# Performance work log

Measured on AMD Instinct MI355X. Metric: run time of the kernel, lower is better.

The kernel has to match this reference:

```python
import jax, jax.numpy as jnp
import numpy as np

TOPK = 5
LAMBDA_ALIGN_K = 16.0
MOM = 0.9          # EMA momentum
DEFAULT_SCORE = 0.5  # EMA bank default (bank starts empty)
EPS = 1e-8
NEG = 1.0e9


def pairwise_cosine(X):
    # torch F.normalize: X / max(||X||, eps)
    n = jnp.linalg.norm(X, axis=-1, keepdims=True)
    Xn = X / jnp.maximum(n, EPS)
    sim = Xn @ Xn.T
    return jnp.clip(sim, -1.0 + EPS, 1.0 - EPS)


def knn_mask(sim, allowed_base, topk=TOPK):
    B = sim.shape[0]
    eye = jnp.eye(B, dtype=sim.dtype)
    allowed = allowed_base * (1.0 - eye)
    masked = sim - NEG * eye
    masked = jnp.where(allowed < 0.5, -NEG, masked)
    masked = jnp.where(masked < 0.0, -NEG, masked)
    cand = (masked > 0).sum(axis=1)
    k = min(topk, max(B - 1, 1))
    keep_row = (cand >= topk).astype(sim.dtype)
    keep = keep_row[:, None] * keep_row[None, :]
    idx = jax.lax.top_k(masked, k)[1]                       # [B, k]
    M = jnp.zeros_like(sim).at[jnp.arange(B)[:, None], idx].set(1.0)
    M = jnp.maximum(M, M.T)
    return M * allowed * keep


def build_intra(sim, same, topk=TOPK):
    M = knn_mask(sim, same, topk)
    A = jnp.maximum(sim * M, 0.0) * same
    return A, M


def pga_loss(feats_sub, labels_sub):
    # feats_sub: [L, b, d]
    L = feats_sub.shape[0]
    same = (labels_sub[:, None] == labels_sub[None, :]).astype(jnp.float32)
    sims = jax.vmap(pairwise_cosine)(feats_sub)             # [L, b, b]
    A, M = jax.vmap(lambda s: build_intra(s, same))(sims)   # [L, b, b] each

    # EMA degree-based scores (no-grad in original; bank starts empty so
    # fetch-after-update == mom*default + (1-mom)*score_cur)
    S_intra = jnp.maximum(sims * same, 0.0)
    deg = jnp.maximum((S_intra > 0).sum(axis=2).astype(jnp.float32), 1.0)
    score_cur = jax.nn.sigmoid(S_intra.sum(axis=2) / deg)   # [L, b]
    ema = jax.lax.stop_gradient(MOM * DEFAULT_SCORE + (1.0 - MOM) * score_cur)

    # layer-pair masked MSE alignment, target detached
    A_deep = A[1:]
    A_tgt = jax.lax.stop_gradient(A[:-1])
    M_eff = jnp.maximum(M[:-1], M[1:])                      # [L-1, b, b]
    W = ema[:-1, :, None] * ema[:-1, None, :]               # [L-1, b, b]
    diff2 = (A_deep - A_tgt) ** 2 * W
    num = (diff2 * M_eff).sum(axis=(1, 2))
    den = jnp.maximum((M_eff * W).sum(axis=(1, 2)), EPS)
    terms = jnp.where(M_eff.sum(axis=(1, 2)) > 0, num / den, 0.0)
    raw = terms.sum() / max(L - 1, 1)
    return LAMBDA_ALIGN_K * raw


def setup_inputs() -> dict:
    key = jax.random.key(0)
    k1, k2 = jax.random.split(key)
    feats_final = jax.random.normal(k1, (8, 2048, 512), dtype=jnp.float32)
    labels = jax.random.randint(k2, (2048,), 0, 128).astype(jnp.int64)
    sample_ids = jnp.arange(2048, dtype=jnp.int64)
    return {"feats_final": feats_final, "labels": labels, "sample_ids": sample_ids}


def reference(feats_final, labels, sample_ids):
    # candidate subset from last layer (no-grad in original)
    X_last = feats_final[-1]
    S_last = pairwise_cosine(X_last)
    same_full = (labels[:, None] == labels[None, :]).astype(jnp.float32)
    _, M_last = build_intra(S_last, same_full)
    cand_mask = (M_last > 0).sum(axis=1) > 0
    idx_sub = jnp.nonzero(cand_mask)[0]  # eager (concrete) subselection
    feats_sub = feats_final[:, idx_sub]  # [L, b, d]
    labels_sub = labels[idx_sub]
    return pga_loss(feats_sub, labels_sub)
```

## Files before the change

kernel.cpp:

```cpp
#include <hip/hip_runtime.h>
#include <cmath>

#define NB   2048
#define ND   512
#define NL   8
#define NLAB 128
#define MAXM 64
#define TOPK_ 5
#define NTH  256
#define MAXSLOT 9
#define GSTRIDE (MAXM*MAXM)

#define SLOT_DECL(s) int off##s = -1; int lds##s = 0; float4 pre##s;
#define SLOT_INIT(s) { int idx = tid + (s)*NTH; if (idx < (m << 5)) { \
    int i = idx >> 5, k4 = idx & 31; \
    off##s = (g_s[i] << 9) + (k4 << 2); \
    lds##s = i * 132 + (k4 << 2); \
    pre##s = *(const float4*)(X + off##s); } }
#define SLOT_STORE(s) if (off##s >= 0) *(float4*)(XtF + lds##s) = pre##s;
#define SLOT_FETCH(s, kcn) if (off##s >= 0) pre##s = *(const float4*)(X + off##s + (kcn));

__global__ __launch_bounds__(NTH) void k_gram(
    const float* __restrict__ feats, const int* __restrict__ labels,
    float* __restrict__ G, int* __restrict__ cnt,
    unsigned long long* __restrict__ insub)
{
    __shared__ int wsum[4];
    __shared__ int g_s[MAXM];
    __shared__ float Xt[MAXM][132];
    __shared__ float rinvp[64];
    __shared__ unsigned long long tops_s[64];
    __shared__ unsigned char keep_s[64];
    float* XtF = &Xt[0][0];
    int c = blockIdx.x, l = blockIdx.y, tid = threadIdx.x;
    int lane = tid & 63, wv = tid >> 6;

    int my[8]; int n = 0; int base_i = tid * 8;
    for (int t = 0; t < 8; ++t) {
        int i = base_i + t;
        if (labels[i] == c) my[n++] = i;
    }
    int scan = n;
    #pragma unroll
    for (int off = 1; off < 64; off <<= 1) {
        int v = __shfl_up(scan, off);
        if (lane >= off) scan += v;
    }
    if (lane == 63) wsum[wv] = scan;
    __syncthreads();
    int w0 = wsum[0], w1 = wsum[1], w2 = wsum[2], w3 = wsum[3];
    int m = w0 + w1 + w2 + w3; if (m > MAXM) m = MAXM;
    int base = (wv > 0 ? w0 : 0) + (wv > 1 ? w1 : 0) + (wv > 2 ? w2 : 0);
    int excl = base + scan - n;
    for (int t = 0; t < n; ++t) {
        int slot = excl + t;
        if (slot < MAXM) g_s[slot] = my[t];
    }
    if (l == 0 && tid == 0) cnt[c] = m;
    __syncthreads();
    if (m == 0) {
        if (l == 7 && tid == 0) insub[c] = 0ull;
        return;
    }

    const float* X = feats + (size_t)l * NB * ND;

    SLOT_DECL(0) SLOT_DECL(1) SLOT_DECL(2) SLOT_DECL(3)
    SLOT_DECL(4) SLOT_DECL(5) SLOT_DECL(6) SLOT_DECL(7)
    SLOT_INIT(0) SLOT_INIT(1) SLOT_INIT(2) SLOT_INIT(3)
    SLOT_INIT(4) SLOT_INIT(5) SLOT_INIT(6) SLOT_INIT(7)

    const int P = m * (m + 1) / 2;
    float acc0[MAXSLOT], acc1[MAXSLOT];
    short is_[MAXSLOT], js_[MAXSLOT];
    int ns = 0;
    for (int p = tid; p < P; p += NTH) {
        int i = (int)((sqrtf(8.0f * (float)p + 1.0f) - 1.0f) * 0.5f);
        while (((i + 1) * (i + 2)) / 2 <= p) ++i;
        while ((i * (i + 1)) / 2 > p) --i;
        is_[ns] = (short)i;
        js_[ns] = (short)(p - (i * (i + 1)) / 2);
        acc0[ns] = 0.0f; acc1[ns] = 0.0f;
        ++ns;
    }

    for (int kc = 0; kc < ND; kc += 128) {
        if (kc) __syncthreads();
        SLOT_STORE(0) SLOT_STORE(1) SLOT_STORE(2) SLOT_STORE(3)
        SLOT_STORE(4) SLOT_STORE(5) SLOT_STORE(6) SLOT_STORE(7)
        __syncthreads();
        if (kc + 128 < ND) {
            int kcn = kc + 128;
            SLOT_FETCH(0, kcn) SLOT_FETCH(1, kcn) SLOT_FETCH(2, kcn) SLOT_FETCH(3, kcn)
            SLOT_FETCH(4, kcn) SLOT_FETCH(5, kcn) SLOT_FETCH(6, kcn) SLOT_FETCH(7, kcn)
        }
        for (int s = 0; s < ns; ++s) {
            int i = is_[s], j = js_[s];
            float a0 = acc0[s], a1 = acc1[s];
            #pragma unroll
            for (int k4 = 0; k4 < 32; ++k4) {
                float4 a = *(const float4*)&Xt[i][k4 << 2];
                float4 b = *(const float4*)&Xt[j][k4 << 2];
                a0 = fmaf(a.x, b.x, a0); a1 = fmaf(a.y, b.y, a1);
                a0 = fmaf(a.z, b.z, a0); a1 = fmaf(a.w, b.w, a1);
            }
            acc0[s] = a0; acc1[s] = a1;
        }
    }

    float (*Gs)[65] = (float(*)[65])(&Xt[0][0]);
    __syncthreads();
    for (int s = 0; s < ns; ++s) {
        int i = is_[s], j = js_[s];
        float v = acc0[s] + acc1[s];
        Gs[i][j] = v; Gs[j][i] = v;
    }
    if (tid < m) for (int j = m; j < 64; ++j) Gs[tid][j] = -2.0f;
    __syncthreads();
    if (tid < 64) rinvp[tid] = (tid < m) ? 1.0f / fmaxf(sqrtf(Gs[tid][tid]), 1e-8f) : 0.0f;
    __syncthreads();
    for (int idx = tid; idx < (m << 6); idx += NTH) {
        int i = idx >> 6, j = idx & 63;
        if (j < m) {
            float raw = Gs[i][j];
            Gs[i][j] = fminf(fmaxf(raw * rinvp[i] * rinvp[j], -1.0f), 1.0f);
        }
    }
    __syncthreads();
    float* Gc = G + ((size_t)l * NLAB + c) * GSTRIDE;
    for (int idx4 = tid; idx4 < (m << 4); idx4 += NTH) {
        int i = idx4 >> 4, j0 = (idx4 & 15) << 2;
        *(float4*)(Gc + i * MAXM + j0) = *(const float4*)&Gs[i][j0];
    }
    if (l != 7) return;

    if (tid < 64) { keep_s[tid] = 0; tops_s[tid] = 0ull; }
    __syncthreads();
    unsigned long long tops = 0ull; bool keep = false;
    if (tid < m) {
        float v0=-1.f,v1=-1.f,v2=-1.f,v3=-1.f,v4=-1.f;
        int i0=0,i1=0,i2=0,i3=0,i4=0, cand=0;
        #pragma unroll 8
        for (int j = 0; j < 64; ++j) {
            float v = Gs[tid][j];
            if (v > 0.0f && j != tid) {
                ++cand;
                if      (v > v0) { v4=v3;i4=i3; v3=v2;i3=i2; v2=v1;i2=i1; v1=v0;i1=i0; v0=v;i0=j; }
                else if (v > v1) { v4=v3;i4=i3; v3=v2;i3=i2; v2=v1;i2=i1; v1=v;i1=j; }
                else if (v > v2) { v4=v3;i4=i3; v3=v2;i3=i2; v2=v;i2=j; }
                else if (v > v3) { v4=v3;i4=i3; v3=v;i3=j; }
                else if (v > v4) { v4=v;i4=j; }
            }
        }
        keep = (cand >= TOPK_);
        if (keep) tops = (1ull<<i0)|(1ull<<i1)|(1ull<<i2)|(1ull<<i3)|(1ull<<i4);
        keep_s[tid] = keep ? 1 : 0; tops_s[tid] = tops;
    }
    __syncthreads();
    unsigned long long Mrow = 0ull;
    if (tid < m && keep) {
        for (int j = 0; j < 64; ++j) {
            if (j == tid || !keep_s[j]) continue;
            if (((tops >> j) & 1ull) || ((tops_s[j] >> tid) & 1ull)) Mrow |= (1ull << j);
        }
    }
    if (tid < 64) {
        unsigned long long b = __ballot(Mrow != 0ull);
        if (tid == 0) insub[c] = b;
    }
}

__global__ __launch_bounds__(NTH) void k_pairdec(
    const float* __restrict__ G, const int* __restrict__ cnt,
    const unsigned long long* __restrict__ insub,
    float* __restrict__ partial)
{
    __shared__ float Gs0[64][65];
    __shared__ float Gs1[64][65];
    __shared__ unsigned long long tops0[64], tops1[64];
    __shared__ unsigned char keep0[64], keep1[64];
    __shared__ unsigned long long M0s[64], M1s[64];
    __shared__ float es[64];
    __shared__ float red[12];
    int c = blockIdx.x, p = blockIdx.y, tid = threadIdx.x;
    int lane = tid & 63, wv = tid >> 6;
    int m = cnt[c]; if (m > MAXM) m = MAXM;
    unsigned long long sub = insub[c];

    const float* G0 = G + ((size_t)p       * NLAB + c) * GSTRIDE;
    const float* G1 = G + ((size_t)(p + 1) * NLAB + c) * GSTRIDE;
    for (int idx4 = tid; idx4 < (m << 4); idx4 += NTH) {
        int i = idx4 >> 4, j0 = (idx4 & 15) << 2;
        *(float4*)&Gs0[i][j0] = *(const float4*)(G0 + i * MAXM + j0);
        *(float4*)&Gs1[i][j0] = *(const float4*)(G1 + i * MAXM + j0);
    }
    if (tid < 64)       { keep0[tid] = 0; tops0[tid] = 0ull; }
    else if (tid < 128) { keep1[tid - 64] = 0; tops1[tid - 64] = 0ull; }
    __syncthreads();

    unsigned long long tops = 0ull; bool keep = false;
    if (wv < 2 && lane < m) {
        const float (*Gt)[65] = (wv == 0) ? Gs0 : Gs1;
        bool act = (sub >> lane) & 1ull;
        float emaval = 0.0f;
        if (act) {
            float v0=-1.f,v1=-1.f,v2=-1.f,v3=-1.f,v4=-1.f;
            int i0=0,i1=0,i2=0,i3=0,i4=0, cand=0, dg=0;
            float rs = 0.0f;
            #pragma unroll 8
            for (int j = 0; j < 64; ++j) {
                float v = Gt[lane][j];
                if (!((sub >> j) & 1ull)) v = -2.0f;
                if (v > 0.0f) {
                    rs += v; ++dg;
                    if (j != lane) {
                        ++cand;
                        if      (v > v0) { v4=v3;i4=i3; v3=v2;i3=i2; v2=v1;i2=i1; v1=v0;i1=i0; v0=v;i0=j; }
                        else if (v > v1) { v4=v3;i4=i3; v3=v2;i3=i2; v2=v1;i2=i1; v1=v;i1=j; }
                        else if (v > v2) { v4=v3;i4=i3; v3=v2;i3=i2; v2=v;i2=j; }
                        else if (v > v3) { v4=v3;i4=i3; v3=v;i3=j; }
                        else if (v > v4) { v4=v;i4=j; }
                    }
                }
            }
            keep = (cand >= TOPK_);
            if (keep) tops = (1ull<<i0)|(1ull<<i1)|(1ull<<i2)|(1ull<<i3)|(1ull<<i4);
            float deg = (float)(dg > 0 ? dg : 1);
            float score = 1.0f / (1.0f + expf(-rs / deg));
            emaval = 0.45f + 0.1f * score;
        }
        if (wv == 0) { keep0[lane] = keep ? 1 : 0; tops0[lane] = tops; es[lane] = emaval; }
        else         { keep1[lane] = keep ? 1 : 0; tops1[lane] = tops; }
    }
    __syncthreads();
    if (wv < 2 && lane < m) {
        const unsigned long long* topsW = (wv == 0) ? tops0 : tops1;
        const unsigned char*     keepW = (wv == 0) ? keep0 : keep1;
        unsigned long long Mrow = 0ull;
        if (keep) {
            for (int j = 0; j < 64; ++j) {
                if (j == lane || !keepW[j]) continue;
                if (((tops >> j) & 1ull) || ((topsW[j] >> lane) & 1ull)) Mrow |= (1ull << j);
            }
        }
        if (wv == 0) M0s[lane] = Mrow; else M1s[lane] = Mrow;
    }
    __syncthreads();

    float fn = 0.0f, fd = 0.0f, fc = 0.0f;
    for (int idx = tid; idx < (m << 6); idx += NTH) {
        int i = idx >> 6, j = idx & 63;
        if (j >= m) continue;
        bool b0 = (M0s[i] >> j) & 1ull;
        bool b1 = (M1s[i] >> j) & 1ull;
        if (b0 | b1) {
            float v0 = b0 ? Gs0[i][j] : 0.0f;
            float v1 = b1 ? Gs1[i][j] : 0.0f;
            float w = es[i] * es[j];
            float d = v1 - v0;
            fn = fmaf(d * d, w, fn);
            fd += w;
            fc += 1.0f;
        }
    }
    for (int off = 32; off > 0; off >>= 1) {
        fn += __shfl_down(fn, off);
        fd += __shfl_down(fd, off);
        fc += __shfl_down(fc, off);
    }
    if ((tid & 63) == 0) { red[wv * 3] = fn; red[wv * 3 + 1] = fd; red[wv * 3 + 2] = fc; }
    __syncthreads();
    if (tid == 0) {
        float* dst = partial + ((size_t)p * NLAB + c) * 4;
        dst[0] = red[0] + red[3] + red[6] + red[9];
        dst[1] = red[1] + red[4] + red[7] + red[10];
        dst[2] = red[2] + red[5] + red[8] + red[11];
    }
}

__global__ void k_final(const float* __restrict__ partial, float* __restrict__ out)
{
    int tid = threadIdx.x;
    float total = 0.0f;
    for (int p = 0; p < NL - 1; ++p) {
        float n = 0.0f, d = 0.0f, cc = 0.0f;
        for (int c = tid; c < NLAB; c += 64) {
            const float* src = partial + ((size_t)p * NLAB + c) * 4;
            n += src[0]; d += src[1]; cc += src[2];
        }
        for (int off = 32; off > 0; off >>= 1) {
            n += __shfl_down(n, off);
            d += __shfl_down(d, off);
            cc += __shfl_down(cc, off);
        }
        if (tid == 0 && cc > 0.0f) total += n / fmaxf(d, 1e-8f);
    }
    if (tid == 0) out[0] = 16.0f * total / 7.0f;
}

extern "C" void kernel_launch(void* const* d_in, const int* in_sizes, int n_in,
                              void* d_out, int out_size, void* d_ws, size_t ws_size,
                              hipStream_t stream) {
    const float* feats  = (const float*)d_in[0];
    const int*   labels = (const int*)d_in[1];
    char* w = (char*)d_ws;
    size_t gbytes = (size_t)NL * NLAB * GSTRIDE * 4;
    float*    G       = (float*)(w);
    float*    partial = (float*)(w + gbytes);
    int*      cnt     = (int*)(w + gbytes + 14336);
    unsigned long long* insub = (unsigned long long*)(w + gbytes + 14848);
    float*    out     = (float*)d_out;

    k_gram   <<<dim3(NLAB, NL),     NTH, 0, stream>>>(feats, labels, G, cnt, insub);
    k_pairdec<<<dim3(NLAB, NL - 1), NTH, 0, stream>>>(G, cnt, insub, partial);
    k_final  <<<1, 64, 0, stream>>>(partial, out);
}
```

Baseline: 129.3 us.

## Fuse gram, pair-decode and final reduction into one kernel via atomic counters

Merges the three kernels into a single launch. The last-arriving layer block per label, detected through a global atomic counter, performs the per-label layer-pair loss serially over all 8 layers, and the last label block does the final reduction. This removes two kernel launches and their gaps, at the cost of serialising the pair work per label on one block (7 pairs instead of 7 parallel blocks) plus fences and atomics.

```diff
diff --git a/kernel.cpp b/kernel.cpp
--- a/kernel.cpp
+++ b/kernel.cpp
@@ -11,6 +11,10 @@
 #define MAXSLOT 9
 #define GSTRIDE (MAXM*MAXM)
 
+
+__device__ unsigned g_done[NLAB * 16];
+__device__ unsigned g_fin;
+
 #define SLOT_DECL(s) int off##s = -1; int lds##s = 0; float4 pre##s;
 #define SLOT_INIT(s) { int idx = tid + (s)*NTH; if (idx < (m << 5)) { \
     int i = idx >> 5, k4 = idx & 31; \
@@ -20,10 +24,10 @@
 #define SLOT_STORE(s) if (off##s >= 0) *(float4*)(XtF + lds##s) = pre##s;
 #define SLOT_FETCH(s, kcn) if (off##s >= 0) pre##s = *(const float4*)(X + off##s + (kcn));
 
-__global__ __launch_bounds__(NTH) void k_gram(
+__global__ __launch_bounds__(NTH) void k_gramfan(
     const float* __restrict__ feats, const int* __restrict__ labels,
-    float* __restrict__ G, int* __restrict__ cnt,
-    unsigned long long* __restrict__ insub)
+    float* __restrict__ G, unsigned long long* __restrict__ insub,
+    float* __restrict__ partial, float* __restrict__ out)
 {
     __shared__ int wsum[4];
     __shared__ int g_s[MAXM];
@@ -31,6 +35,10 @@
     __shared__ float rinvp[64];
     __shared__ unsigned long long tops_s[64];
     __shared__ unsigned char keep_s[64];
+    __shared__ unsigned long long Ml[NL][64];
+    __shared__ float El[NL][64];
+    __shared__ float red[12];
+    __shared__ int sh_prev;
     float* XtF = &Xt[0][0];
     int c = blockIdx.x, l = blockIdx.y, tid = threadIdx.x;
     int lane = tid & 63, wv = tid >> 6;
@@ -56,164 +64,90 @@
         int slot = excl + t;
         if (slot < MAXM) g_s[slot] = my[t];
     }
-    if (l == 0 && tid == 0) cnt[c] = m;
-    __syncthreads();
-    if (m == 0) {
-        if (l == 7 && tid == 0) insub[c] = 0ull;
-        return;
-    }
-
-    const float* X = feats + (size_t)l * NB * ND;
-
-    SLOT_DECL(0) SLOT_DECL(1) SLOT_DECL(2) SLOT_DECL(3)
-    SLOT_DECL(4) SLOT_DECL(5) SLOT_DECL(6) SLOT_DECL(7)
-    SLOT_INIT(0) SLOT_INIT(1) SLOT_INIT(2) SLOT_INIT(3)
-    SLOT_INIT(4) SLOT_INIT(5) SLOT_INIT(6) SLOT_INIT(7)
-
-    const int P = m * (m + 1) / 2;
-    float acc0[MAXSLOT], acc1[MAXSLOT];
-    short is_[MAXSLOT], js_[MAXSLOT];
-    int ns = 0;
-    for (int p = tid; p < P; p += NTH) {
-        int i = (int)((sqrtf(8.0f * (float)p + 1.0f) - 1.0f) * 0.5f);
-        while (((i + 1) * (i + 2)) / 2 <= p) ++i;
-        while ((i * (i + 1)) / 2 > p) --i;
-        is_[ns] = (short)i;
-        js_[ns] = (short)(p - (i * (i + 1)) / 2);
-        acc0[ns] = 0.0f; acc1[ns] = 0.0f;
-        ++ns;
-    }
-
-    for (int kc = 0; kc < ND; kc += 128) {
-        if (kc) __syncthreads();
-        SLOT_STORE(0) SLOT_STORE(1) SLOT_STORE(2) SLOT_STORE(3)
-        SLOT_STORE(4) SLOT_STORE(5) SLOT_STORE(6) SLOT_STORE(7)
-        __syncthreads();
-        if (kc + 128 < ND) {
-            int kcn = kc + 128;
-            SLOT_FETCH(0, kcn) SLOT_FETCH(1, kcn) SLOT_FETCH(2, kcn) SLOT_FETCH(3, kcn)
-            SLOT_FETCH(4, kcn) SLOT_FETCH(5, kcn) SLOT_FETCH(6, kcn) SLOT_FETCH(7, kcn)
-        }
+    __syncthreads();
+
+    if (m > 0) {
+        const float* X = feats + (size_t)l * NB * ND;
+
+        SLOT_DECL(0) SLOT_DECL(1) SLOT_DECL(2) SLOT_DECL(3)
+        SLOT_DECL(4) SLOT_DECL(5) SLOT_DECL(6) SLOT_DECL(7)
+        SLOT_INIT(0) SLOT_INIT(1) SLOT_INIT(2) SLOT_INIT(3)
+        SLOT_INIT(4) SLOT_INIT(5) SLOT_INIT(6) SLOT_INIT(7)
+
+        const int P = m * (m + 1) / 2;
+        float acc0[MAXSLOT], acc1[MAXSLOT];
+        short is_[MAXSLOT], js_[MAXSLOT];
+        int ns = 0;
+        for (int p = tid; p < P; p += NTH) {
+            int i = (int)((sqrtf(8.0f * (float)p + 1.0f) - 1.0f) * 0.5f);
+            while (((i + 1) * (i + 2)) / 2 <= p) ++i;
+            while ((i * (i + 1)) / 2 > p) --i;
+            is_[ns] = (short)i;
+            js_[ns] = (short)(p - (i * (i + 1)) / 2);
+            acc0[ns] = 0.0f; acc1[ns] = 0.0f;
+            ++ns;
+        }
+
+        for (int kc = 0; kc < ND; kc += 128) {
+            if (kc) __syncthreads();
+            SLOT_STORE(0) SLOT_STORE(1) SLOT_STORE(2) SLOT_STORE(3)
+            SLOT_STORE(4) SLOT_STORE(5) SLOT_STORE(6) SLOT_STORE(7)
+            __syncthreads();
+            if (kc + 128 < ND) {
+                int kcn = kc + 128;
+                SLOT_FETCH(0, kcn) SLOT_FETCH(1, kcn) SLOT_FETCH(2, kcn) SLOT_FETCH(3, kcn)
+                SLOT_FETCH(4, kcn) SLOT_FETCH(5, kcn) SLOT_FETCH(6, kcn) SLOT_FETCH(7, kcn)
+            }
+            for (int s = 0; s < ns; ++s) {
+                int i = is_[s], j = js_[s];
+                float a0 = acc0[s], a1 = acc1[s];
+                #pragma unroll
+                for (int k4 = 0; k4 < 32; ++k4) {
+                    float4 a = *(const float4*)&Xt[i][k4 << 2];
+                    float4 b = *(const float4*)&Xt[j][k4 << 2];
+                    a0 = fmaf(a.x, b.x, a0); a1 = fmaf(a.y, b.y, a1);
+                    a0 = fmaf(a.z, b.z, a0); a1 = fmaf(a.w, b.w, a1);
+                }
+                acc0[s] = a0; acc1[s] = a1;
+            }
+        }
+
+        float (*Gs)[65] = (float(*)[65])(&Xt[0][0]);
+        __syncthreads();
         for (int s = 0; s < ns; ++s) {
             int i = is_[s], j = js_[s];
-            float a0 = acc0[s], a1 = acc1[s];
-            #pragma unroll
-            for (int k4 = 0; k4 < 32; ++k4) {
-                float4 a = *(const float4*)&Xt[i][k4 << 2];
-                float4 b = *(const float4*)&Xt[j][k4 << 2];
-                a0 = fmaf(a.x, b.x, a0); a1 = fmaf(a.y, b.y, a1);
-                a0 = fmaf(a.z, b.z, a0); a1 = fmaf(a.w, b.w, a1);
-            }
-            acc0[s] = a0; acc1[s] = a1;
-        }
-    }
-
-    float (*Gs)[65] = (float(*)[65])(&Xt[0][0]);
-    __syncthreads();
-    for (int s = 0; s < ns; ++s) {
-        int i = is_[s], j = js_[s];
-        float v = acc0[s] + acc1[s];
-        Gs[i][j] = v; Gs[j][i] = v;
-    }
-    if (tid < m) for (int j = m; j < 64; ++j) Gs[tid][j] = -2.0f;
-    __syncthreads();
-    if (tid < 64) rinvp[tid] = (tid < m) ? 1.0f / fmaxf(sqrtf(Gs[tid][tid]), 1e-8f) : 0.0f;
-    __syncthreads();
-    for (int idx = tid; idx < (m << 6); idx += NTH) {
-        int i = idx >> 6, j = idx & 63;
-        if (j < m) {
-            float raw = Gs[i][j];
-            Gs[i][j] = fminf(fmaxf(raw * rinvp[i] * rinvp[j], -1.0f), 1.0f);
-        }
-    }
-    __syncthreads();
-    float* Gc = G + ((size_t)l * NLAB + c) * GSTRIDE;
-    for (int idx4 = tid; idx4 < (m << 4); idx4 += NTH) {
-        int i = idx4 >> 4, j0 = (idx4 & 15) << 2;
-        *(float4*)(Gc + i * MAXM + j0) = *(const float4*)&Gs[i][j0];
-    }
-    if (l != 7) return;
-
-    if (tid < 64) { keep_s[tid] = 0; tops_s[tid] = 0ull; }
-    __syncthreads();
-    unsigned long long tops = 0ull; bool keep = false;
-    if (tid < m) {
-        float v0=-1.f,v1=-1.f,v2=-1.f,v3=-1.f,v4=-1.f;
-        int i0=0,i1=0,i2=0,i3=0,i4=0, cand=0;
-        #pragma unroll 8
-        for (int j = 0; j < 64; ++j) {
-            float v = Gs[tid][j];
-            if (v > 0.0f && j != tid) {
-                ++cand;
-                if      (v > v0) { v4=v3;i4=i3; v3=v2;i3=i2; v2=v1;i2=i1; v1=v0;i1=i0; v0=v;i0=j; }
-                else if (v > v1) { v4=v3;i4=i3; v3=v2;i3=i2; v2=v1;i2=i1; v1=v;i1=j; }
-                else if (v > v2) { v4=v3;i4=i3; v3=v2;i3=i2; v2=v;i2=j; }
-                else if (v > v3) { v4=v3;i4=i3; v3=v;i3=j; }
-                else if (v > v4) { v4=v;i4=j; }
-            }
-        }
-        keep = (cand >= TOPK_);
-        if (keep) tops = (1ull<<i0)|(1ull<<i1)|(1ull<<i2)|(1ull<<i3)|(1ull<<i4);
-        keep_s[tid] = keep ? 1 : 0; tops_s[tid] = tops;
-    }
-    __syncthreads();
-    unsigned long long Mrow = 0ull;
-    if (tid < m && keep) {
-        for (int j = 0; j < 64; ++j) {
-            if (j == tid || !keep_s[j]) continue;
-            if (((tops >> j) & 1ull) || ((tops_s[j] >> tid) & 1ull)) Mrow |= (1ull << j);
-        }
-    }
-    if (tid < 64) {
-        unsigned long long b = __ballot(Mrow != 0ull);
-        if (tid == 0) insub[c] = b;
-    }
-}
-
-__global__ __launch_bounds__(NTH) void k_pairdec(
-    const float* __restrict__ G, const int* __restrict__ cnt,
-    const unsigned long long* __restrict__ insub,
-    float* __restrict__ partial)
-{
-    __shared__ float Gs0[64][65];
-    __shared__ float Gs1[64][65];
-    __shared__ unsigned long long tops0[64], tops1[64];
-    __shared__ unsigned char keep0[64], keep1[64];
-    __shared__ unsigned long long M0s[64], M1s[64];
-    __shared__ float es[64];
-    __shared__ float red[12];
-    int c = blockIdx.x, p = blockIdx.y, tid = threadIdx.x;
-    int lane = tid & 63, wv = tid >> 6;
-    int m = cnt[c]; if (m > MAXM) m = MAXM;
-    unsigned long long sub = insub[c];
-
-    const float* G0 = G + ((size_t)p       * NLAB + c) * GSTRIDE;
-    const float* G1 = G + ((size_t)(p + 1) * NLAB + c) * GSTRIDE;
-    for (int idx4 = tid; idx4 < (m << 4); idx4 += NTH) {
-        int i = idx4 >> 4, j0 = (idx4 & 15) << 2;
-        *(float4*)&Gs0[i][j0] = *(const float4*)(G0 + i * MAXM + j0);
-        *(float4*)&Gs1[i][j0] = *(const float4*)(G1 + i * MAXM + j0);
-    }
-    if (tid < 64)       { keep0[tid] = 0; tops0[tid] = 0ull; }
-    else if (tid < 128) { keep1[tid - 64] = 0; tops1[tid - 64] = 0ull; }
-    __syncthreads();
-
-    unsigned long long tops = 0ull; bool keep = false;
-    if (wv < 2 && lane < m) {
-        const float (*Gt)[65] = (wv == 0) ? Gs0 : Gs1;
-        bool act = (sub >> lane) & 1ull;
-        float emaval = 0.0f;
-        if (act) {
-            float v0=-1.f,v1=-1.f,v2=-1.f,v3=-1.f,v4=-1.f;
-            int i0=0,i1=0,i2=0,i3=0,i4=0, cand=0, dg=0;
-            float rs = 0.0f;
-            #pragma unroll 8
-            for (int j = 0; j < 64; ++j) {
-                float v = Gt[lane][j];
-                if (!((sub >> j) & 1ull)) v = -2.0f;
-                if (v > 0.0f) {
-                    rs += v; ++dg;
-                    if (j != lane) {
+            float v = acc0[s] + acc1[s];
+            Gs[i][j] = v; Gs[j][i] = v;
+        }
+        if (tid < m) for (int j = m; j < 64; ++j) Gs[tid][j] = -2.0f;
+        __syncthreads();
+        if (tid < 64) rinvp[tid] = (tid < m) ? 1.0f / fmaxf(sqrtf(Gs[tid][tid]), 1e-8f) : 0.0f;
+        __syncthreads();
+        for (int idx = tid; idx < (m << 6); idx += NTH) {
+            int i = idx >> 6, j = idx & 63;
+            if (j < m) {
+                float raw = Gs[i][j];
+                Gs[i][j] = fminf(fmaxf(raw * rinvp[i] * rinvp[j], -1.0f), 1.0f);
+            }
+        }
+        __syncthreads();
+        float* Gc = G + ((size_t)l * NLAB + c) * GSTRIDE;
+        for (int idx4 = tid; idx4 < (m << 4); idx4 += NTH) {
+            int i = idx4 >> 4, j0 = (idx4 & 15) << 2;
+            *(float4*)(Gc + i * MAXM + j0) = *(const float4*)&Gs[i][j0];
+        }
+
+        if (l == 7) {
+            if (tid < 64) { keep_s[tid] = 0; tops_s[tid] = 0ull; }
+            __syncthreads();
+            unsigned long long tops = 0ull; bool keep = false;
+            if (tid < m) {
+                float v0=-1.f,v1=-1.f,v2=-1.f,v3=-1.f,v4=-1.f;
+                int i0=0,i1=0,i2=0,i3=0,i4=0, cand=0;
+                #pragma unroll 8
+                for (int j = 0; j < 64; ++j) {
+                    float v = Gs[tid][j];
+                    if (v > 0.0f && j != tid) {
                         ++cand;
                         if      (v > v0) { v4=v3;i4=i3; v3=v2;i3=i2; v2=v1;i2=i1; v1=v0;i1=i0; v0=v;i0=j; }
                         else if (v > v1) { v4=v3;i4=i3; v3=v2;i3=i2; v2=v1;i2=i1; v1=v;i1=j; }
@@ -222,80 +156,168 @@
                         else if (v > v4) { v4=v;i4=j; }
                     }
                 }
-            }
-            keep = (cand >= TOPK_);
-            if (keep) tops = (1ull<<i0)|(1ull<<i1)|(1ull<<i2)|(1ull<<i3)|(1ull<<i4);
-            float deg = (float)(dg > 0 ? dg : 1);
-            float score = 1.0f / (1.0f + expf(-rs / deg));
-            emaval = 0.45f + 0.1f * score;
-        }
-        if (wv == 0) { keep0[lane] = keep ? 1 : 0; tops0[lane] = tops; es[lane] = emaval; }
-        else         { keep1[lane] = keep ? 1 : 0; tops1[lane] = tops; }
-    }
-    __syncthreads();
-    if (wv < 2 && lane < m) {
-        const unsigned long long* topsW = (wv == 0) ? tops0 : tops1;
-        const unsigned char*     keepW = (wv == 0) ? keep0 : keep1;
-        unsigned long long Mrow = 0ull;
-        if (keep) {
-            for (int j = 0; j < 64; ++j) {
-                if (j == lane || !keepW[j]) continue;
-                if (((tops >> j) & 1ull) || ((topsW[j] >> lane) & 1ull)) Mrow |= (1ull << j);
-            }
-        }
-        if (wv == 0) M0s[lane] = Mrow; else M1s[lane] = Mrow;
-    }
-    __syncthreads();
-
-    float fn = 0.0f, fd = 0.0f, fc = 0.0f;
-    for (int idx = tid; idx < (m << 6); idx += NTH) {
-        int i = idx >> 6, j = idx & 63;
-        if (j >= m) continue;
-        bool b0 = (M0s[i] >> j) & 1ull;
-        bool b1 = (M1s[i] >> j) & 1ull;
-        if (b0 | b1) {
-            float v0 = b0 ? Gs0[i][j] : 0.0f;
-            float v1 = b1 ? Gs1[i][j] : 0.0f;
-            float w = es[i] * es[j];
-            float d = v1 - v0;
-            fn = fmaf(d * d, w, fn);
-            fd += w;
-            fc += 1.0f;
-        }
-    }
-    for (int off = 32; off > 0; off >>= 1) {
-        fn += __shfl_down(fn, off);
-        fd += __shfl_down(fd, off);
-        fc += __shfl_down(fc, off);
-    }
-    if ((tid & 63) == 0) { red[wv * 3] = fn; red[wv * 3 + 1] = fd; red[wv * 3 + 2] = fc; }
+                keep = (cand >= TOPK_);
+                if (keep) tops = (1ull<<i0)|(1ull<<i1)|(1ull<<i2)|(1ull<<i3)|(1ull<<i4);
+                keep_s[tid] = keep ? 1 : 0; tops_s[tid] = tops;
+            }
+            __syncthreads();
+            unsigned long long Mrow = 0ull;
+            if (tid < m && keep) {
+                for (int j = 0; j < 64; ++j) {
+                    if (j == tid || !keep_s[j]) continue;
+                    if (((tops >> j) & 1ull) || ((tops_s[j] >> tid) & 1ull)) Mrow |= (1ull << j);
+                }
+            }
+            if (tid < 64) {
+                unsigned long long b = __ballot(Mrow != 0ull);
+                if (tid == 0) insub[c] = b;
+            }
+        }
+    } else {
+        if (l == 7 && tid == 0) insub[c] = 0ull;
+    }
+
+    __threadfence();
     __syncthreads();
     if (tid == 0) {
-        float* dst = partial + ((size_t)p * NLAB + c) * 4;
-        dst[0] = red[0] + red[3] + red[6] + red[9];
-        dst[1] = red[1] + red[4] + red[7] + red[10];
-        dst[2] = red[2] + red[5] + red[8] + red[11];
-    }
-}
-
-__global__ void k_final(const float* __restrict__ partial, float* __restrict__ out)
-{
-    int tid = threadIdx.x;
-    float total = 0.0f;
-    for (int p = 0; p < NL - 1; ++p) {
-        float n = 0.0f, d = 0.0f, cc = 0.0f;
-        for (int c = tid; c < NLAB; c += 64) {
-            const float* src = partial + ((size_t)p * NLAB + c) * 4;
-            n += src[0]; d += src[1]; cc += src[2];
-        }
-        for (int off = 32; off > 0; off >>= 1) {
-            n += __shfl_down(n, off);
-            d += __shfl_down(d, off);
-            cc += __shfl_down(cc, off);
-        }
-        if (tid == 0 && cc > 0.0f) total += n / fmaxf(d, 1e-8f);
-    }
-    if (tid == 0) out[0] = 16.0f * total / 7.0f;
+        unsigned prev = __hip_atomic_fetch_add(&g_done[c * 16], 1u,
+                            __ATOMIC_ACQ_REL, __HIP_MEMORY_SCOPE_AGENT);
+        sh_prev = (int)prev;
+        if (prev == NL - 1)
+            __hip_atomic_store(&g_done[c * 16], 0u, __ATOMIC_RELAXED, __HIP_MEMORY_SCOPE_AGENT);
+    }
+    __syncthreads();
+    if (sh_prev != NL - 1) return;
+    __threadfence();
+
+    float (*B0)[65] = (float(*)[65])(XtF);
+    float (*B1)[65] = (float(*)[65])(XtF + 4160);
+    unsigned long long sub = insub[c];
+
+    for (int lp = 0; lp < NL; ++lp) {
+        float (*Gt)[65] = (lp & 1) ? B1 : B0;
+        const float* Gl = G + ((size_t)lp * NLAB + c) * GSTRIDE;
+        __syncthreads();
+        for (int idx4 = tid; idx4 < (m << 4); idx4 += NTH) {
+            int i = idx4 >> 4, j0 = (idx4 & 15) << 2;
+            *(float4*)&Gt[i][j0] = *(const float4*)(Gl + i * MAXM + j0);
+        }
+        if (tid < 64) { keep_s[tid] = 0; tops_s[tid] = 0ull; }
+        __syncthreads();
+
+        unsigned long long tops = 0ull; bool keep = false;
+        if (wv == 0 && lane < m) {
+            bool act = (sub >> lane) & 1ull;
+            float emaval = 0.0f;
+            if (act) {
+                float v0=-1.f,v1=-1.f,v2=-1.f,v3=-1.f,v4=-1.f;
+                int i0=0,i1=0,i2=0,i3=0,i4=0, cand=0, dg=0;
+                float rs = 0.0f;
+                #pragma unroll 8
+                for (int j = 0; j < 64; ++j) {
+                    float v = Gt[lane][j];
+                    if (!((sub >> j) & 1ull)) v = -2.0f;
+                    if (v > 0.0f) {
+                        rs += v; ++dg;
+                        if (j != lane) {
+                            ++cand;
+                            if      (v > v0) { v4=v3;i4=i3; v3=v2;i3=i2; v2=v1;i2=i1; v1=v0;i1=i0; v0=v;i0=j; }
+                            else if (v > v1) { v4=v3;i4=i3; v3=v2;i3=i2; v2=v1;i2=i1; v1=v;i1=j; }
+                            else if (v > v2) { v4=v3;i4=i3; v3=v2;i3=i2; v2=v;i2=j; }
+                            else if (v > v3) { v4=v3;i4=i3; v3=v;i3=j; }
+                            else if (v > v4) { v4=v;i4=j; }
+                        }
+                    }
+                }
+                keep = (cand >= TOPK_);
+                if (keep) tops = (1ull<<i0)|(1ull<<i1)|(1ull<<i2)|(1ull<<i3)|(1ull<<i4);
+                float deg = (float)(dg > 0 ? dg : 1);
+                float score = 1.0f / (1.0f + expf(-rs / deg));
+                emaval = 0.45f + 0.1f * score;
+            }
+            keep_s[lane] = keep ? 1 : 0; tops_s[lane] = tops;
+            El[lp][lane] = emaval;
+        }
+        __syncthreads();
+        if (wv == 0 && lane < m) {
+            unsigned long long Mrow = 0ull;
+            if (keep) {
+                for (int j = 0; j < 64; ++j) {
+                    if (j == lane || !keep_s[j]) continue;
+                    if (((tops >> j) & 1ull) || ((tops_s[j] >> lane) & 1ull)) Mrow |= (1ull << j);
+                }
+            }
+            Ml[lp][lane] = Mrow;
+        }
+        __syncthreads();
+
+        if (lp >= 1) {
+            int p = lp - 1;
+            const float (*Bp)[65]  = (p & 1) ? B1 : B0;
+            const float (*Bp1)[65] = (p & 1) ? B0 : B1;
+            float fn = 0.0f, fd = 0.0f, fc = 0.0f;
+            for (int idx = tid; idx < (m << 6); idx += NTH) {
+                int i = idx >> 6, j = idx & 63;
+                if (j >= m) continue;
+                bool b0 = (Ml[p][i] >> j) & 1ull;
+                bool b1 = (Ml[p + 1][i] >> j) & 1ull;
+                if (b0 | b1) {
+                    float v0 = b0 ? Bp[i][j] : 0.0f;
+                    float v1 = b1 ? Bp1[i][j] : 0.0f;
+                    float w = El[p][i] * El[p][j];
+                    float d = v1 - v0;
+                    fn = fmaf(d * d, w, fn);
+                    fd += w;
+                    fc += 1.0f;
+                }
+            }
+            for (int off = 32; off > 0; off >>= 1) {
+                fn += __shfl_down(fn, off);
+                fd += __shfl_down(fd, off);
+                fc += __shfl_down(fc, off);
+            }
+            if ((tid & 63) == 0) { red[wv * 3] = fn; red[wv * 3 + 1] = fd; red[wv * 3 + 2] = fc; }
+            __syncthreads();
+            if (tid == 0) {
+                float* dst = partial + ((size_t)p * NLAB + c) * 4;
+                dst[0] = red[0] + red[3] + red[6] + red[9];
+                dst[1] = red[1] + red[4] + red[7] + red[10];
+                dst[2] = red[2] + red[5] + red[8] + red[11];
+            }
+            __syncthreads();
+        }
+    }
+
+    __threadfence();
+    __syncthreads();
+    if (tid == 0) {
+        unsigned pf = __hip_atomic_fetch_add(&g_fin, 1u,
+                          __ATOMIC_ACQ_REL, __HIP_MEMORY_SCOPE_AGENT);
+        sh_prev = (int)pf;
+        if (pf == NLAB - 1)
+            __hip_atomic_store(&g_fin, 0u, __ATOMIC_RELAXED, __HIP_MEMORY_SCOPE_AGENT);
+    }
+    __syncthreads();
+    if (sh_prev != NLAB - 1) return;
+    __threadfence();
+
+    if (tid < 64) {
+        float total = 0.0f;
+        for (int p = 0; p < NL - 1; ++p) {
+            float nn = 0.0f, d = 0.0f, cc = 0.0f;
+            for (int ci = tid; ci < NLAB; ci += 64) {
+                const float* src = partial + ((size_t)p * NLAB + ci) * 4;
+                nn += src[0]; d += src[1]; cc += src[2];
+            }
+            for (int off = 32; off > 0; off >>= 1) {
+                nn += __shfl_down(nn, off);
+                d += __shfl_down(d, off);
+                cc += __shfl_down(cc, off);
+            }
+            if (tid == 0 && cc > 0.0f) total += nn / fmaxf(d, 1e-8f);
+        }
+        if (tid == 0) out[0] = 16.0f * total / 7.0f;
+    }
 }
 
 extern "C" void kernel_launch(void* const* d_in, const int* in_sizes, int n_in,
@@ -307,11 +329,8 @@
     size_t gbytes = (size_t)NL * NLAB * GSTRIDE * 4;
     float*    G       = (float*)(w);
     float*    partial = (float*)(w + gbytes);
-    int*      cnt     = (int*)(w + gbytes + 14336);
-    unsigned long long* insub = (unsigned long long*)(w + gbytes + 14848);
+    unsigned long long* insub = (unsigned long long*)(w + gbytes + 14336 + 512);
     float*    out     = (float*)d_out;
 
-    k_gram   <<<dim3(NLAB, NL),     NTH, 0, stream>>>(feats, labels, G, cnt, insub);
-    k_pairdec<<<dim3(NLAB, NL - 1), NTH, 0, stream>>>(G, cnt, insub, partial);
-    k_final  <<<1, 64, 0, stream>>>(partial, out);
+    k_gramfan<<<dim3(NLAB, NL), NTH, 0, stream>>>(feats, labels, G, insub, partial, out);
 }
```

After: 323.2 us. +150.0%, slower.
